# Performance work log

Measured on AMD Instinct MI355X. Metric: run time of the kernel, lower is better.

## Reference

```python
import jax, jax.numpy as jnp
import numpy as np

EPS = 1e-6
BETA = 0.25

def _l2_normalize(x, axis=-1):
    # matches torch F.normalize(p=2, eps=1e-6): x / max(||x||, eps)
    n = jnp.sqrt(jnp.sum(x * x, axis=axis, keepdims=True))
    return x / jnp.maximum(n, EPS)

def setup_inputs() -> dict:
    key = jax.random.key(0)
    k1, k2 = jax.random.split(key)
    h = jax.random.normal(k1, (32, 1024, 512), dtype=jnp.float32)
    codebook = jax.random.normal(k2, (1024, 512), dtype=jnp.float32)
    # module normalizes codebook rows at init
    codebook = _l2_normalize(codebook, axis=1)
    return {"h": h, "codebook": codebook, "training": 0}

def reference(h, codebook, training):
    B, T, D = h.shape
    K = codebook.shape[0]
    h_flat = h.reshape(-1, D)                      # [N, D]
    h_norm = _l2_normalize(h_flat, axis=1)         # [N, D]
    cb = _l2_normalize(codebook, axis=1)           # [K, D]
    # squared L2 distances: ||h||^2 + ||c||^2 - 2 h.c (equivalent to cdist**2)
    h_sq = jnp.sum(h_norm * h_norm, axis=1, keepdims=True)        # [N, 1]
    c_sq = jnp.sum(cb * cb, axis=1)[None, :]                      # [1, K]
    distances = h_sq + c_sq - 2.0 * (h_norm @ cb.T)               # [N, K]
    # eval path: hard one-hot assignment via argmin
    indices_flat = jnp.argmin(distances, axis=1)                  # [N]
    q_flat = jax.nn.one_hot(indices_flat, K, dtype=distances.dtype)  # [N, K]
    c_tilde_flat = q_flat @ cb                                    # [N, D]
    c_hard_flat = cb[indices_flat]                                # [N, D]
    diff = h_norm - c_tilde_flat
    codebook_loss = jnp.mean(jax.lax.stop_gradient(diff) ** 2)
    commitment_loss = jnp.mean(diff ** 2)
    q = q_flat.reshape(B, T, K)
    c_tilde = c_tilde_flat.reshape(B, T, D)
    c_hard = c_hard_flat.reshape(B, T, D)
    # straight-through: forward = c_hard, grads flow through c_tilde and c_hard
    c_quantized = c_tilde + (c_hard - jax.lax.stop_gradient(c_tilde))
    loss = codebook_loss + BETA * commitment_loss
    return (q, c_tilde, c_hard, c_quantized, loss, indices_flat)
```

## Files before the change

### kernel.cpp

```cpp
#include <hip/hip_runtime.h>
#include <math.h>


#define NROWS 32768
#define DDIM  512
#define KCODE 1024
#define MARGIN_COEF 0.017f

typedef __attribute__((address_space(1))) const void gvoid_t;
typedef __attribute__((address_space(3))) void svoid_t;
typedef float f32x4 __attribute__((ext_vector_type(4)));
typedef short bf16x8 __attribute__((ext_vector_type(8)));

__device__ __forceinline__ void gl16(const void* g, void* s) {
  __builtin_amdgcn_global_load_lds((gvoid_t*)g, (svoid_t*)s, 16, 0, 0);
}
__device__ __forceinline__ unsigned short f2bf(float x) {
  unsigned u = __float_as_uint(x);
  u = u + 0x7fffu + ((u >> 16) & 1u);
  return (unsigned short)(u >> 16);
}

__global__ __launch_bounds__(256) void k_invc(const float* __restrict__ x,
                                              double* __restrict__ invd,
                                              float* __restrict__ invf,
                                              float* __restrict__ cbn) {
  const int lane = threadIdx.x & 63;
  const int row = blockIdx.x * 4 + (threadIdx.x >> 6);
  const float* p = x + (size_t)row * DDIM;
  float4 v0 = *(const float4*)(p + lane * 4);
  float4 v1 = *(const float4*)(p + 256 + lane * 4);
  double s = (double)v0.x * v0.x + (double)v0.y * v0.y + (double)v0.z * v0.z + (double)v0.w * v0.w
           + (double)v1.x * v1.x + (double)v1.y * v1.y + (double)v1.z * v1.z + (double)v1.w * v1.w;
  #pragma unroll
  for (int m = 1; m < 64; m <<= 1) s += __shfl_xor(s, m);
  const double iv = 1.0 / fmax(sqrt(s), 1e-6);
  float4 n0, n1;
  n0.x = (float)((double)v0.x * iv); n0.y = (float)((double)v0.y * iv);
  n0.z = (float)((double)v0.z * iv); n0.w = (float)((double)v0.w * iv);
  n1.x = (float)((double)v1.x * iv); n1.y = (float)((double)v1.y * iv);
  n1.z = (float)((double)v1.z * iv); n1.w = (float)((double)v1.w * iv);
  *(float4*)(cbn + (size_t)row * DDIM + lane * 4) = n0;
  *(float4*)(cbn + (size_t)row * DDIM + 256 + lane * 4) = n1;
  if (lane == 0) {
    invd[row] = iv;
    invf[row] = (float)iv;
  }
}

__global__ __launch_bounds__(256) void k_prep(const float* __restrict__ src,
                                              unsigned short* __restrict__ hi,
                                              float* __restrict__ nrm) {
  const int tile = blockIdx.x;
  const int t = threadIdx.x;
  const int r = t >> 4;
  const int l16 = t & 15;
  const float4* s4 = (const float4*)(src + (size_t)tile * 16 * DDIM);
  double ss = 0.0;
  #pragma unroll
  for (int j = 0; j < 8; ++j) {
    const int f4 = r * 128 + l16 + j * 16;
    float4 v = s4[f4];
    ss += (double)v.x * v.x + (double)v.y * v.y + (double)v.z * v.z + (double)v.w * v.w;
    const int k = (l16 + j * 16) * 4;
    const int kc = k >> 5;
    const int l = r | (((k >> 3) & 3) << 4);
    ushort4 h4;
    h4.x = f2bf(v.x); h4.y = f2bf(v.y); h4.z = f2bf(v.z); h4.w = f2bf(v.w);
    *(ushort4*)(hi + (size_t)tile * 8192 + kc * 512 + l * 8 + (k & 7)) = h4;
  }
  #pragma unroll
  for (int m = 1; m < 16; m <<= 1) ss += __shfl_xor(ss, m);
  if (l16 == 0) nrm[tile * 16 + r] = (float)sqrt(ss);
}

__global__ __launch_bounds__(256) void k_mfma(const unsigned short* __restrict__ AThi,
                                              const unsigned short* __restrict__ BThi,
                                              const float* __restrict__ invcf,
                                              const float* __restrict__ hnormf,
                                              float4* __restrict__ pcand,
                                              int* __restrict__ pt3) {
  __shared__ bf16x8 lds[2048];
  const int tx = threadIdx.x;
  const int bid = blockIdx.x;
  const int pr = (bid & 7) * 32 + (bid >> 6);
  const int pc = (bid >> 3) & 7;
  const int lane = tx & 63;
  const int wid = tx >> 6;
  const int wr = wid >> 1, wc = wid & 1;

  f32x4 acc[4][4];
  #pragma unroll
  for (int m = 0; m < 4; ++m)
    #pragma unroll
    for (int n = 0; n < 4; ++n) acc[m][n] = (f32x4)(0.0f);

  const size_t aA0 = (size_t)(pr * 8 + wid) * 8192 + lane * 8;
  const size_t aA1 = (size_t)(pr * 8 + wid + 4) * 8192 + lane * 8;
  const size_t aB0 = (size_t)(pc * 8 + wid) * 8192 + lane * 8;
  const size_t aB1 = (size_t)(pc * 8 + wid + 4) * 8192 + lane * 8;
  const int slA0 = wid * 64 + lane;
  const int slA1 = (wid + 4) * 64 + lane;
  const int slB0 = 512 + wid * 64 + lane;
  const int slB1 = 512 + (wid + 4) * 64 + lane;

#define STAGE(bufi, kcc)                                   \
  {                                                        \
    bf16x8* base = &lds[(bufi) * 1024];                    \
    const int o_ = (kcc) * 512;                            \
    gl16(AThi + aA0 + o_, base + slA0);                    \
    gl16(AThi + aA1 + o_, base + slA1);                    \
    gl16(BThi + aB0 + o_, base + slB0);                    \
    gl16(BThi + aB1 + o_, base + slB1);                    \
  }

  STAGE(0, 0);
  __syncthreads();

  for (int kc = 0; kc < 16; ++kc) {
    if (kc < 15) STAGE((kc + 1) & 1, kc + 1);
    const bf16x8* L = &lds[(kc & 1) * 1024];
    bf16x8 af[4], bq[4];
    #pragma unroll
    for (int m = 0; m < 4; ++m) af[m] = L[(wr * 4 + m) * 64 + lane];
    #pragma unroll
    for (int n = 0; n < 4; ++n) bq[n] = L[512 + (wc * 4 + n) * 64 + lane];
    #pragma unroll
    for (int m = 0; m < 4; ++m)
      #pragma unroll
      for (int n = 0; n < 4; ++n)
        acc[m][n] = __builtin_amdgcn_mfma_f32_16x16x32_bf16(af[m], bq[n], acc[m][n], 0, 0, 0);
    __syncthreads();
  }
#undef STAGE

  const int q = lane >> 4;
  const int c16 = lane & 15;
  const int rowbase = pr * 128 + wr * 64;
  const int colbase = pc * 128 + wc * 64;
  const int st = colbase >> 6;

  float invn[4];
  #pragma unroll
  for (int n4 = 0; n4 < 4; ++n4) invn[n4] = invcf[colbase + n4 * 16 + c16];

  #pragma unroll
  for (int m = 0; m < 4; ++m) {
    #pragma unroll
    for (int r = 0; r < 4; ++r) {
      const int row = rowbase + m * 16 + q * 4 + r;
      float sv[4];
      #pragma unroll
      for (int n4 = 0; n4 < 4; ++n4) sv[n4] = acc[m][n4][r] * invn[n4];

      float t1 = sv[0]; int i1 = colbase + c16;
      #pragma unroll
      for (int n4 = 1; n4 < 4; ++n4) {
        const int idx = colbase + n4 * 16 + c16;
        if (sv[n4] > t1) { t1 = sv[n4]; i1 = idx; }
      }
      #pragma unroll
      for (int msk = 1; msk < 16; msk <<= 1) {
        float os = __shfl_xor(t1, msk); int oi = __shfl_xor(i1, msk);
        if (os > t1 || (os == t1 && oi < i1)) { t1 = os; i1 = oi; }
      }

      float t2 = -3.4e38f; int i2 = 0x7fffffff;
      #pragma unroll
      for (int n4 = 0; n4 < 4; ++n4) {
        const int idx = colbase + n4 * 16 + c16;
        if (idx != i1 && sv[n4] > t2) { t2 = sv[n4]; i2 = idx; }
      }
      #pragma unroll
      for (int msk = 1; msk < 16; msk <<= 1) {
        float os = __shfl_xor(t2, msk); int oi = __shfl_xor(i2, msk);
        if (os > t2 || (os == t2 && oi < i2)) { t2 = os; i2 = oi; }
      }

      float t3 = -3.4e38f;
      #pragma unroll
      for (int n4 = 0; n4 < 4; ++n4) {
        const int idx = colbase + n4 * 16 + c16;
        if (idx != i1 && idx != i2 && sv[n4] > t3) t3 = sv[n4];
      }
      #pragma unroll
      for (int msk = 1; msk < 16; msk <<= 1)
        t3 = fmaxf(t3, __shfl_xor(t3, msk));

      if (c16 == 0) {
        pcand[(size_t)row * 16 + st] = make_float4(t1, __int_as_float(i1), t2, __int_as_float(i2));
        pt3[(size_t)row * 16 + st] = __float_as_int(t3);
      }
    }
  }
}

__global__ __launch_bounds__(256) void k_select(const float* __restrict__ h,
                                                const float* __restrict__ cb,
                                                const double* __restrict__ invcd,
                                                const float* __restrict__ hnormf,
                                                const float4* __restrict__ pcand,
                                                const int* __restrict__ pt3,
                                                int* __restrict__ sidxb,
                                                float* __restrict__ out_idx) {
  const int lane = threadIdx.x & 63;
  const int row = blockIdx.x * 4 + (threadIdx.x >> 6);

  float4 pc4 = make_float4(-3.4e38f, 0.0f, -3.4e38f, 0.0f);
  float t3 = -3.4e38f;
  if (lane < 16) {
    pc4 = pcand[(size_t)row * 16 + lane];
    t3 = __int_as_float(pt3[(size_t)row * 16 + lane]);
  }
  float best = pc4.x;
  #pragma unroll
  for (int m = 1; m < 64; m <<= 1) best = fmaxf(best, __shfl_xor(best, m));
  const float thr = best - MARGIN_COEF * hnormf[row];

  const unsigned long long m1 = __ballot(pc4.x >= thr);
  const unsigned long long m2 = __ballot(pc4.z >= thr);
  const unsigned long long mr = __ballot(t3 >= thr);

  const float4* hp = (const float4*)(h + (size_t)row * DDIM + lane * 8);
  const float4 h0 = hp[0], h1 = hp[1];

  double bs = -1e300; int bi = 0x7fffffff;
  const int i1 = __float_as_int(pc4.y);
  const int i2 = __float_as_int(pc4.w);

  #define RESCORE(codeexpr)                                                  \
    {                                                                        \
      const int code = (codeexpr);                                           \
      const float4* cp = (const float4*)(cb + (size_t)code * DDIM + lane*8); \
      const float4 c0 = cp[0], c1 = cp[1];                                   \
      double p = (double)h0.x * c0.x + (double)h0.y * c0.y                   \
               + (double)h0.z * c0.z + (double)h0.w * c0.w                   \
               + (double)h1.x * c1.x + (double)h1.y * c1.y                   \
               + (double)h1.z * c1.z + (double)h1.w * c1.w;                  \
      _Pragma("unroll")                                                      \
      for (int m = 1; m < 64; m <<= 1) p += __shfl_xor(p, m);                \
      const double sc = p * invcd[code];                                     \
      if (sc > bs || (sc == bs && code < bi)) { bs = sc; bi = code; }        \
    }

  for (unsigned long long mm = m1; mm; mm &= mm - 1)
    RESCORE(__shfl(i1, __builtin_ctzll(mm)));
  for (unsigned long long mm = m2; mm; mm &= mm - 1)
    RESCORE(__shfl(i2, __builtin_ctzll(mm)));
  for (unsigned long long mm = mr; mm; mm &= mm - 1) {
    const int st = __builtin_ctzll(mm);
    for (int j = 0; j < 64; ++j) RESCORE(st * 64 + j);
  }
  #undef RESCORE

  if (lane == 0) {
    sidxb[row] = bi;
    out_idx[row] = (float)bi;
  }
}

__global__ __launch_bounds__(256) void k_write(const float* __restrict__ h,
                                               const float* __restrict__ cbn,
                                               const int* __restrict__ sidxb,
                                               float* __restrict__ out_q,
                                               float* __restrict__ out_ct,
                                               float* __restrict__ out_ch,
                                               float* __restrict__ out_cq,
                                               double* __restrict__ lsum) {
  const int tx = threadIdx.x;
  const int r = blockIdx.x * 8 + (tx >> 5);
  const int g = tx & 31;
  const int bi = sidxb[r];

  {
    float* qrow = out_q + (size_t)r * KCODE;
    #pragma unroll
    for (int j = 0; j < 8; ++j) {
      const int col = g * 4 + j * 128;
      float4 qv;
      qv.x = (col + 0 == bi) ? 1.0f : 0.0f;
      qv.y = (col + 1 == bi) ? 1.0f : 0.0f;
      qv.z = (col + 2 == bi) ? 1.0f : 0.0f;
      qv.w = (col + 3 == bi) ? 1.0f : 0.0f;
      *(float4*)(qrow + col) = qv;
    }
  }

  float4 hvv[4], cvv[4];
  const float* hrow = h + (size_t)r * DDIM;
  const float* crow = cbn + (size_t)bi * DDIM;
  #pragma unroll
  for (int j = 0; j < 4; ++j) {
    const int col = g * 4 + j * 128;
    hvv[j] = *(const float4*)(hrow + col);
    cvv[j] = *(const float4*)(crow + col);
  }
  double hs = 0.0;
  #pragma unroll
  for (int j = 0; j < 4; ++j)
    hs += (double)hvv[j].x * hvv[j].x + (double)hvv[j].y * hvv[j].y
        + (double)hvv[j].z * hvv[j].z + (double)hvv[j].w * hvv[j].w;
  #pragma unroll
  for (int m = 1; m < 32; m <<= 1) hs += __shfl_xor(hs, m);
  const double ih = 1.0 / fmax(sqrt(hs), 1e-6);

  double ls = 0.0;
  #pragma unroll
  for (int j = 0; j < 4; ++j) {
    const int col = g * 4 + j * 128;
    const size_t ro = (size_t)r * DDIM + col;
    *(float4*)(out_ct + ro) = cvv[j];
    *(float4*)(out_ch + ro) = cvv[j];
    *(float4*)(out_cq + ro) = cvv[j];
    double e;
    e = (double)hvv[j].x * ih - (double)cvv[j].x; ls += e * e;
    e = (double)hvv[j].y * ih - (double)cvv[j].y; ls += e * e;
    e = (double)hvv[j].z * ih - (double)cvv[j].z; ls += e * e;
    e = (double)hvv[j].w * ih - (double)cvv[j].w; ls += e * e;
  }
  #pragma unroll
  for (int m = 1; m < 32; m <<= 1) ls += __shfl_xor(ls, m);
  if (g == 0) lsum[r] = ls;
}

__global__ __launch_bounds__(256) void k_loss(const double* __restrict__ lsum,
                                              float* __restrict__ out_loss) {
  const int tx = threadIdx.x;
  double s = 0.0;
  for (int i = tx; i < NROWS; i += 256) s += lsum[i];
  #pragma unroll
  for (int m = 1; m < 64; m <<= 1) s += __shfl_xor(s, m);
  __shared__ double sh[4];
  if ((tx & 63) == 0) sh[tx >> 6] = s;
  __syncthreads();
  if (tx == 0)
    out_loss[0] = (float)(1.25 * (sh[0] + sh[1] + sh[2] + sh[3]) / ((double)NROWS * (double)DDIM));
}

extern "C" void kernel_launch(void* const* d_in, const int* in_sizes, int n_in,
                              void* d_out, int out_size, void* d_ws, size_t ws_size,
                              hipStream_t stream) {
  const float* h = (const float*)d_in[0];
  const float* cb = (const float*)d_in[1];

  float* out = (float*)d_out;
  float* out_q    = out;
  float* out_ct   = out + 33554432;
  float* out_ch   = out + 50331648;
  float* out_cq   = out + 67108864;
  float* out_loss = out + 83886080;
  float* out_idx  = out + 83886081;

  char* ws = (char*)d_ws;
  unsigned short* AThi = (unsigned short*)(ws);
  unsigned short* BThi = (unsigned short*)(ws + 33554432);
  double* invcd  = (double*)(ws + 34603008);
  float*  invcf  = (float*)(ws + 34611200);
  float*  hnormf = (float*)(ws + 34615296);
  float*  cbnrm  = (float*)(ws + 34746368);
  float*  cbn    = (float*)(ws + 34750464);
  float4* pcand  = (float4*)(ws + 36847616);
  int*    pt3    = (int*)(ws + 45236224);
  double* lsum   = (double*)(ws + 47333376);
  int*    sidxb  = (int*)(ws + 47595520);

  k_invc<<<KCODE / 4, 256, 0, stream>>>(cb, invcd, invcf, cbn);
  k_prep<<<NROWS / 16, 256, 0, stream>>>(h, AThi, hnormf);
  k_prep<<<KCODE / 16, 256, 0, stream>>>(cb, BThi, cbnrm);
  k_mfma<<<2048, 256, 0, stream>>>(AThi, BThi, invcf, hnormf, pcand, pt3);
  k_select<<<NROWS / 4, 256, 0, stream>>>(h, cb, invcd, hnormf, pcand, pt3,
                                          sidxb, out_idx);
  k_write<<<NROWS / 8, 256, 0, stream>>>(h, cbn, sidxb,
                                         out_q, out_ct, out_ch, out_cq, lsum);
  k_loss<<<1, 256, 0, stream>>>(lsum, out_loss);
}
```

Before: 307.3 us.

## Fuse select and write kernels, reuse h row and precomputed norm, nontemporal stores

Merges the candidate rescoring kernel with the output-writing kernel, so each wavefront writes the one-hot, the three codebook copies and the per-row loss right after picking the index. The h row loaded for rescoring is reused for the loss. The h norm is taken from a double-precision value that the prep kernel now stores, instead of being recomputed. Large output writes use nontemporal stores. This removes a kernel launch, a re-read of h, and the index round-trip through global memory. In exchange the write phase now runs at the select kernel's one-wave-per-row shape.

```diff
diff --git a/kernel.cpp b/kernel.cpp
--- a/kernel.cpp
+++ b/kernel.cpp
@@ -50,7 +50,8 @@
 
 __global__ __launch_bounds__(256) void k_prep(const float* __restrict__ src,
                                               unsigned short* __restrict__ hi,
-                                              float* __restrict__ nrm) {
+                                              float* __restrict__ nrmf,
+                                              double* __restrict__ nrmd) {
   const int tile = blockIdx.x;
   const int t = threadIdx.x;
   const int r = t >> 4;
@@ -71,7 +72,11 @@
   }
   #pragma unroll
   for (int m = 1; m < 16; m <<= 1) ss += __shfl_xor(ss, m);
-  if (l16 == 0) nrm[tile * 16 + r] = (float)sqrt(ss);
+  if (l16 == 0) {
+    const double nd = sqrt(ss);
+    nrmf[tile * 16 + r] = (float)nd;
+    nrmd[tile * 16 + r] = nd;
+  }
 }
 
 __global__ __launch_bounds__(256) void k_mfma(const unsigned short* __restrict__ AThi,
@@ -195,14 +200,20 @@
   }
 }
 
-__global__ __launch_bounds__(256) void k_select(const float* __restrict__ h,
-                                                const float* __restrict__ cb,
-                                                const double* __restrict__ invcd,
-                                                const float* __restrict__ hnormf,
-                                                const float4* __restrict__ pcand,
-                                                const int* __restrict__ pt3,
-                                                int* __restrict__ sidxb,
-                                                float* __restrict__ out_idx) {
+__global__ __launch_bounds__(256) void k_selwrite(const float* __restrict__ h,
+                                                  const float* __restrict__ cb,
+                                                  const float* __restrict__ cbn,
+                                                  const double* __restrict__ invcd,
+                                                  const double* __restrict__ hnormd,
+                                                  const float* __restrict__ hnormf,
+                                                  const float4* __restrict__ pcand,
+                                                  const int* __restrict__ pt3,
+                                                  float* __restrict__ out_q,
+                                                  float* __restrict__ out_ct,
+                                                  float* __restrict__ out_ch,
+                                                  float* __restrict__ out_cq,
+                                                  float* __restrict__ out_idx,
+                                                  double* __restrict__ lsum) {
   const int lane = threadIdx.x & 63;
   const int row = blockIdx.x * 4 + (threadIdx.x >> 6);
 
@@ -221,26 +232,28 @@
   const unsigned long long m2 = __ballot(pc4.z >= thr);
   const unsigned long long mr = __ballot(t3 >= thr);
 
-  const float4* hp = (const float4*)(h + (size_t)row * DDIM + lane * 8);
-  const float4 h0 = hp[0], h1 = hp[1];
+  const float* hrow = h + (size_t)row * DDIM;
+  const f32x4 h0 = *(const f32x4*)(hrow + lane * 4);
+  const f32x4 h1 = *(const f32x4*)(hrow + 256 + lane * 4);
 
   double bs = -1e300; int bi = 0x7fffffff;
   const int i1 = __float_as_int(pc4.y);
   const int i2 = __float_as_int(pc4.w);
 
-  #define RESCORE(codeexpr)                                                  \
-    {                                                                        \
-      const int code = (codeexpr);                                           \
-      const float4* cp = (const float4*)(cb + (size_t)code * DDIM + lane*8); \
-      const float4 c0 = cp[0], c1 = cp[1];                                   \
-      double p = (double)h0.x * c0.x + (double)h0.y * c0.y                   \
-               + (double)h0.z * c0.z + (double)h0.w * c0.w                   \
-               + (double)h1.x * c1.x + (double)h1.y * c1.y                   \
-               + (double)h1.z * c1.z + (double)h1.w * c1.w;                  \
-      _Pragma("unroll")                                                      \
-      for (int m = 1; m < 64; m <<= 1) p += __shfl_xor(p, m);                \
-      const double sc = p * invcd[code];                                     \
-      if (sc > bs || (sc == bs && code < bi)) { bs = sc; bi = code; }        \
+  #define RESCORE(codeexpr)                                                   \
+    {                                                                         \
+      const int code = (codeexpr);                                            \
+      const float* cp = cb + (size_t)code * DDIM;                             \
+      const f32x4 c0 = *(const f32x4*)(cp + lane * 4);                        \
+      const f32x4 c1 = *(const f32x4*)(cp + 256 + lane * 4);                  \
+      double p = (double)h0.x * c0.x + (double)h0.y * c0.y                    \
+               + (double)h0.z * c0.z + (double)h0.w * c0.w                    \
+               + (double)h1.x * c1.x + (double)h1.y * c1.y                    \
+               + (double)h1.z * c1.z + (double)h1.w * c1.w;                   \
+      _Pragma("unroll")                                                       \
+      for (int m = 1; m < 64; m <<= 1) p += __shfl_xor(p, m);                 \
+      const double sc = p * invcd[code];                                      \
+      if (sc > bs || (sc == bs && code < bi)) { bs = sc; bi = code; }         \
     }
 
   for (unsigned long long mm = m1; mm; mm &= mm - 1)
@@ -253,74 +266,48 @@
   }
   #undef RESCORE
 
-  if (lane == 0) {
-    sidxb[row] = bi;
-    out_idx[row] = (float)bi;
-  }
-}
-
-__global__ __launch_bounds__(256) void k_write(const float* __restrict__ h,
-                                               const float* __restrict__ cbn,
-                                               const int* __restrict__ sidxb,
-                                               float* __restrict__ out_q,
-                                               float* __restrict__ out_ct,
-                                               float* __restrict__ out_ch,
-                                               float* __restrict__ out_cq,
-                                               double* __restrict__ lsum) {
-  const int tx = threadIdx.x;
-  const int r = blockIdx.x * 8 + (tx >> 5);
-  const int g = tx & 31;
-  const int bi = sidxb[r];
+  if (lane == 0) out_idx[row] = (float)bi;
 
   {
-    float* qrow = out_q + (size_t)r * KCODE;
-    #pragma unroll
-    for (int j = 0; j < 8; ++j) {
-      const int col = g * 4 + j * 128;
-      float4 qv;
+    float* qrow = out_q + (size_t)row * KCODE;
+    #pragma unroll
+    for (int p = 0; p < 4; ++p) {
+      const int col = p * 256 + lane * 4;
+      f32x4 qv;
       qv.x = (col + 0 == bi) ? 1.0f : 0.0f;
       qv.y = (col + 1 == bi) ? 1.0f : 0.0f;
       qv.z = (col + 2 == bi) ? 1.0f : 0.0f;
       qv.w = (col + 3 == bi) ? 1.0f : 0.0f;
-      *(float4*)(qrow + col) = qv;
+      __builtin_nontemporal_store(qv, (f32x4*)(qrow + col));
     }
   }
 
-  float4 hvv[4], cvv[4];
-  const float* hrow = h + (size_t)r * DDIM;
+  const double ih = 1.0 / fmax(hnormd[row], 1e-6);
   const float* crow = cbn + (size_t)bi * DDIM;
-  #pragma unroll
-  for (int j = 0; j < 4; ++j) {
-    const int col = g * 4 + j * 128;
-    hvv[j] = *(const float4*)(hrow + col);
-    cvv[j] = *(const float4*)(crow + col);
-  }
-  double hs = 0.0;
-  #pragma unroll
-  for (int j = 0; j < 4; ++j)
-    hs += (double)hvv[j].x * hvv[j].x + (double)hvv[j].y * hvv[j].y
-        + (double)hvv[j].z * hvv[j].z + (double)hvv[j].w * hvv[j].w;
-  #pragma unroll
-  for (int m = 1; m < 32; m <<= 1) hs += __shfl_xor(hs, m);
-  const double ih = 1.0 / fmax(sqrt(hs), 1e-6);
-
-  double ls = 0.0;
-  #pragma unroll
-  for (int j = 0; j < 4; ++j) {
-    const int col = g * 4 + j * 128;
-    const size_t ro = (size_t)r * DDIM + col;
-    *(float4*)(out_ct + ro) = cvv[j];
-    *(float4*)(out_ch + ro) = cvv[j];
-    *(float4*)(out_cq + ro) = cvv[j];
-    double e;
-    e = (double)hvv[j].x * ih - (double)cvv[j].x; ls += e * e;
-    e = (double)hvv[j].y * ih - (double)cvv[j].y; ls += e * e;
-    e = (double)hvv[j].z * ih - (double)cvv[j].z; ls += e * e;
-    e = (double)hvv[j].w * ih - (double)cvv[j].w; ls += e * e;
-  }
-  #pragma unroll
-  for (int m = 1; m < 32; m <<= 1) ls += __shfl_xor(ls, m);
-  if (g == 0) lsum[r] = ls;
+  const f32x4 c0 = *(const f32x4*)(crow + lane * 4);
+  const f32x4 c1 = *(const f32x4*)(crow + 256 + lane * 4);
+
+  const size_t ro0 = (size_t)row * DDIM + lane * 4;
+  const size_t ro1 = ro0 + 256;
+  __builtin_nontemporal_store(c0, (f32x4*)(out_ct + ro0));
+  __builtin_nontemporal_store(c1, (f32x4*)(out_ct + ro1));
+  __builtin_nontemporal_store(c0, (f32x4*)(out_ch + ro0));
+  __builtin_nontemporal_store(c1, (f32x4*)(out_ch + ro1));
+  __builtin_nontemporal_store(c0, (f32x4*)(out_cq + ro0));
+  __builtin_nontemporal_store(c1, (f32x4*)(out_cq + ro1));
+
+  double ls = 0.0, e;
+  e = (double)h0.x * ih - (double)c0.x; ls += e * e;
+  e = (double)h0.y * ih - (double)c0.y; ls += e * e;
+  e = (double)h0.z * ih - (double)c0.z; ls += e * e;
+  e = (double)h0.w * ih - (double)c0.w; ls += e * e;
+  e = (double)h1.x * ih - (double)c1.x; ls += e * e;
+  e = (double)h1.y * ih - (double)c1.y; ls += e * e;
+  e = (double)h1.z * ih - (double)c1.z; ls += e * e;
+  e = (double)h1.w * ih - (double)c1.w; ls += e * e;
+  #pragma unroll
+  for (int m = 1; m < 64; m <<= 1) ls += __shfl_xor(ls, m);
+  if (lane == 0) lsum[row] = ls;
 }
 
 __global__ __launch_bounds__(256) void k_loss(const double* __restrict__ lsum,
@@ -357,20 +344,21 @@
   double* invcd  = (double*)(ws + 34603008);
   float*  invcf  = (float*)(ws + 34611200);
   float*  hnormf = (float*)(ws + 34615296);
-  float*  cbnrm  = (float*)(ws + 34746368);
+  float*  cbnrmf = (float*)(ws + 34746368);
   float*  cbn    = (float*)(ws + 34750464);
   float4* pcand  = (float4*)(ws + 36847616);
   int*    pt3    = (int*)(ws + 45236224);
   double* lsum   = (double*)(ws + 47333376);
-  int*    sidxb  = (int*)(ws + 47595520);
+  double* hnormd = (double*)(ws + 47595520);
+  double* cbnrmd = (double*)(ws + 47857664);
 
   k_invc<<<KCODE / 4, 256, 0, stream>>>(cb, invcd, invcf, cbn);
-  k_prep<<<NROWS / 16, 256, 0, stream>>>(h, AThi, hnormf);
-  k_prep<<<KCODE / 16, 256, 0, stream>>>(cb, BThi, cbnrm);
+  k_prep<<<NROWS / 16, 256, 0, stream>>>(h, AThi, hnormf, hnormd);
+  k_prep<<<KCODE / 16, 256, 0, stream>>>(cb, BThi, cbnrmf, cbnrmd);
   k_mfma<<<2048, 256, 0, stream>>>(AThi, BThi, invcf, hnormf, pcand, pt3);
-  k_select<<<NROWS / 4, 256, 0, stream>>>(h, cb, invcd, hnormf, pcand, pt3,
-                                          sidxb, out_idx);
-  k_write<<<NROWS / 8, 256, 0, stream>>>(h, cbn, sidxb,
-                                         out_q, out_ct, out_ch, out_cq, lsum);
+  k_selwrite<<<NROWS / 4, 256, 0, stream>>>(h, cb, cbn, invcd, hnormd, hnormf,
+                                            pcand, pt3,
+                                            out_q, out_ct, out_ch, out_cq,
+                                            out_idx, lsum);
   k_loss<<<1, 256, 0, stream>>>(lsum, out_loss);
 }
```

Measured after the change: 275.0 us, median of 2. 1.12x faster.
